# Kernel optimization log

Hardware: AMD Instinct MI355X
Metric: run time of the kernel (lower is better)

Reference implementation:

```python
import jax, jax.numpy as jnp
import numpy as np

GAMMA = 0.96875
ROPE_THETA = 10000.0


def _rope(x):
    # x: (B, S, d) -> rotary applied over interleaved pairs (torchtune-style)
    B, S, d = x.shape
    inv_freq = 1.0 / (ROPE_THETA ** (jnp.arange(0, d, 2, dtype=jnp.float32) / d))  # (d/2,)
    angles = jnp.arange(S, dtype=jnp.float32)[:, None] * inv_freq[None, :]  # (S, d/2)
    cos = jnp.cos(angles).astype(x.dtype)
    sin = jnp.sin(angles).astype(x.dtype)
    xs = x.reshape(B, S, d // 2, 2)
    x0, x1 = xs[..., 0], xs[..., 1]
    out = jnp.stack([x0 * cos - x1 * sin, x1 * cos + x0 * sin], axis=-1)
    return out.reshape(B, S, d)


def _decay_mask(S, dtype):
    n = jnp.arange(S)[:, None]
    m = jnp.arange(S)[None, :]
    diff = n - m
    # gamma^(n-m) for n>=m else 0; clamp exponent to avoid inf/nan
    D = jnp.exp(jnp.maximum(diff, 0).astype(jnp.float32) * np.log(GAMMA))
    return jnp.where(diff >= 0, D, 0.0).astype(dtype)


def setup_inputs() -> dict:
    key = jax.random.key(0)
    k1, k2, k3, k4 = jax.random.split(key, 4)
    H = 256
    X = jax.random.normal(k1, (4, 8192, H), dtype=jnp.float32)
    W_Q = jax.random.normal(k2, (H, H), dtype=jnp.float32) / H
    W_K = jax.random.normal(k3, (H, H), dtype=jnp.float32) / H
    W_V = jax.random.normal(k4, (H, H), dtype=jnp.float32) / H
    return {"X": X, "W_Q": W_Q, "W_K": W_K, "W_V": W_V}


def reference(X, W_Q, W_K, W_V):
    B, S, _ = X.shape
    D = _decay_mask(S, X.dtype)  # (S, S)
    Q = _rope(X @ W_Q)  # (B, S, d)
    K = _rope(X @ W_K)
    V = X @ W_V  # (B, S, v_dim)
    ret = jnp.einsum('bqd,bkd->bqk', Q, K) * D[None]  # (B, S, S)
    return ret @ V
```

## Files before the change

### kernel.cpp

```cpp
#include <hip/hip_runtime.h>
#include <hip/hip_bf16.h>

#define B_  4
#define S_  8192
#define H_  256
#define C_  128
#define NC_ 64
#define M_  (B_*S_)

typedef unsigned short u16;
typedef __attribute__((ext_vector_type(8))) short short8;
typedef __attribute__((ext_vector_type(4))) float f32x4;
typedef __attribute__((address_space(1))) void gas_t;
typedef __attribute__((address_space(3))) void las_t;

static constexpr float L2G   = -0.045803690f;
static constexpr float ROPE2 = -0.103810253f;

__device__ __forceinline__ u16 f2b(float x) {
  union { __hip_bfloat16 b; u16 u; } c; c.b = __float2bfloat16(x); return c.u;
}
__device__ __forceinline__ float b2f(u16 u) {
  union { u16 u; __hip_bfloat16 b; } c; c.u = u; return __bfloat162float(c.b);
}
__device__ __forceinline__ f32x4 mfma16(short8 a, short8 b, f32x4 c) {
  return __builtin_amdgcn_mfma_f32_16x16x32_bf16(a, b, c, 0, 0, 0);
}

__device__ __forceinline__ short8 fr32(const u16* base, int row, int slot) {
  return *reinterpret_cast<const short8*>(base + row*256 + (((slot&24)|((slot&7)^(row&7)))<<3));
}
__device__ __forceinline__ short8 fr16(const u16* base, int row, int slot) {
  return *reinterpret_cast<const short8*>(base + row*128 + (((slot&8)|((slot&7)^(row&7)))<<3));
}
__device__ __forceinline__ short8 fr4(const u16* base, int row, int slot) {
  return *reinterpret_cast<const short8*>(base + row*32 + ((slot ^ (row&3))<<3));
}
__device__ __forceinline__ short8 fragr(const u16* lds, int row, int slot) {
  return *reinterpret_cast<const short8*>(lds + row*64 + ((slot ^ (row & 7)) << 3));
}

__device__ __forceinline__ void stageA(const u16* __restrict__ src, int stride,
                                       u16* smbase, int off, int t) {
  #pragma unroll
  for (int it = 0; it < 4; ++it) {
    const int u = it*256 + t, row = u >> 3, lsl = (u & 7) ^ (row & 7);
    const u16* gp = src + (size_t)row*stride + lsl*8;
    u16* lp = smbase + off + it*2048 + (t & 192)*8;
    __builtin_amdgcn_global_load_lds((gas_t*)gp, (las_t*)lp, 16, 0, 0);
  }
}
__device__ __forceinline__ void stageW(const u16* __restrict__ src, u16* dst, int t) {
  #pragma unroll
  for (int it = 0; it < 2; ++it) {
    const int u = it*512 + t, row = u >> 2, p = u & 3, s = p ^ (row & 3);
    const u16* gp = src + (size_t)row*256 + s*8;
    u16* lp = dst + (size_t)(it*512 + (t & ~63))*8;
    __builtin_amdgcn_global_load_lds((gas_t*)gp, (las_t*)lp, 16, 0, 0);
  }
}

__global__ __launch_bounds__(256) void prep(
    const float* __restrict__ Wq, const float* __restrict__ Wk,
    const float* __restrict__ Wv, u16* __restrict__ WhT, float* __restrict__ RTab)
{
  const int bid = blockIdx.x;
  if (bid < 96) {
    const int i = bid*256 + threadIdx.x;
    const int z = i >> 13, r = i & 8191;
    const int n = r >> 5, k0 = (r & 31) << 3;
    const float* W = (z == 0) ? Wq : (z == 1) ? Wk : Wv;
    u16 o[8];
    #pragma unroll
    for (int j = 0; j < 8; ++j) o[j] = f2b(W[(size_t)(k0 + j)*H_ + n]);
    *reinterpret_cast<uint4*>(WhT + ((size_t)z << 16) + n*H_ + k0) =
        *reinterpret_cast<uint4*>(o);
    return;
  }
  const int i = (bid - 96)*256 + threadIdx.x;
  const int s = i >> 7, h = i & 127;
  const float invf = exp2f(ROPE2 * (float)h);
  float sn, cs;
  sincosf((float)s * invf, &sn, &cs);
  *reinterpret_cast<float2*>(RTab + 2*((size_t)s*128 + h)) = make_float2(cs, sn);
}

__global__ __launch_bounds__(512, 2) void fused_chunk(
    const float* __restrict__ X, const u16* __restrict__ WhT,
    const float* __restrict__ RTab,
    u16* __restrict__ Qh, u16* __restrict__ Tt, float* __restrict__ Oloc)
{
  __shared__ u16 SM[81920];
  u16* XS = SM;
  u16* WB = SM + 32768;
  u16* RB = SM + 49152;
  const int t = threadIdx.x, l = t & 63, wid = t >> 6;
  const int g = l >> 4, l15 = l & 15;
  const int mr = wid >> 2, nq = wid & 3;
  const int c = blockIdx.x, b = blockIdx.y;
  const float* Xc = X + ((size_t)(b*S_ + c*C_))*H_;
  const float4* RT4 = reinterpret_cast<const float4*>(RTab);

  stageW(WhT + 0, WB, t);
  #pragma unroll
  for (int it = 0; it < 8; ++it) {
    const int u = it*512 + t, row = u >> 5, sl = u & 31;
    const float* p = Xc + (size_t)row*256 + sl*8;
    float4 a = *reinterpret_cast<const float4*>(p);
    float4 bb = *reinterpret_cast<const float4*>(p + 4);
    u16 o[8] = {f2b(a.x), f2b(a.y), f2b(a.z), f2b(a.w),
                f2b(bb.x), f2b(bb.y), f2b(bb.z), f2b(bb.w)};
    *reinterpret_cast<uint4*>(XS + row*256 + (((sl&24)|((sl&7)^(row&7)))<<3)) =
        *reinterpret_cast<uint4*>(o);
  }
  __syncthreads();

  f32x4 qa[4][4] = {};
  for (int ks = 0; ks < 8; ++ks) {
    const u16* Wcur = WB + (ks&1)*8192;
    if (ks < 7) stageW(WhT + (ks+1)*32, WB + ((ks+1)&1)*8192, t);
    short8 a[4], bw[4];
    #pragma unroll
    for (int i = 0; i < 4; ++i) a[i] = fr32(XS, mr*64 + i*16 + l15, ks*4 + g);
    #pragma unroll
    for (int j = 0; j < 4; ++j) bw[j] = fr4(Wcur, nq*64 + j*16 + l15, g);
    #pragma unroll
    for (int i = 0; i < 4; ++i)
      #pragma unroll
      for (int j = 0; j < 4; ++j)
        qa[i][j] = mfma16(bw[j], a[i], qa[i][j]);
    __syncthreads();
  }
  #pragma unroll
  for (int i = 0; i < 4; ++i) {
    const int s = c*C_ + mr*64 + i*16 + l15;
    #pragma unroll
    for (int j = 0; j < 4; ++j) {
      const int n0 = nq*64 + j*16 + g*4;
      const float4 tb = RT4[(size_t)s*64 + (n0 >> 2)];
      const float x0 = qa[i][j][0], x1 = qa[i][j][1];
      const float x2 = qa[i][j][2], x3 = qa[i][j][3];
      qa[i][j][0] = x0*tb.x - x1*tb.y;  qa[i][j][1] = x1*tb.x + x0*tb.y;
      qa[i][j][2] = x2*tb.z - x3*tb.w;  qa[i][j][3] = x3*tb.z + x2*tb.w;
    }
  }
  #pragma unroll
  for (int i = 0; i < 4; ++i) {
    const int m = mr*64 + i*16 + l15;
    #pragma unroll
    for (int j = 0; j < 4; ++j) {
      const int n0 = nq*64 + j*16 + g*4;
      ushort4 pk;
      pk.x = f2b(qa[i][j][0]); pk.y = f2b(qa[i][j][1]);
      pk.z = f2b(qa[i][j][2]); pk.w = f2b(qa[i][j][3]);
      const int sl = n0 >> 3;
      *reinterpret_cast<ushort4*>(RB + m*256 + (((sl&24)|((sl&7)^(m&7)))<<3) + (n0&7)) = pk;
    }
  }
  __syncthreads();
  #pragma unroll
  for (int it = 0; it < 8; ++it) {
    const int u = it*512 + t, row = u >> 5, sl = u & 31;
    uint4 v = *reinterpret_cast<const uint4*>(RB + row*256 + (((sl&24)|((sl&7)^(row&7)))<<3));
    *reinterpret_cast<uint4*>(Qh + ((size_t)(b*S_ + c*C_ + row))*H_ + sl*8) = v;
  }

  f32x4 ka[4][4] = {};
  stageW(WhT + 65536, WB, t);
  __syncthreads();
  for (int ks = 0; ks < 8; ++ks) {
    const u16* Wcur = WB + (ks&1)*8192;
    if (ks < 7) stageW(WhT + 65536 + (ks+1)*32, WB + ((ks+1)&1)*8192, t);
    short8 a[4], bw[4];
    #pragma unroll
    for (int i = 0; i < 4; ++i) a[i] = fr32(XS, mr*64 + i*16 + l15, ks*4 + g);
    #pragma unroll
    for (int j = 0; j < 4; ++j) bw[j] = fr4(Wcur, nq*64 + j*16 + l15, g);
    #pragma unroll
    for (int i = 0; i < 4; ++i)
      #pragma unroll
      for (int j = 0; j < 4; ++j)
        ka[i][j] = mfma16(bw[j], a[i], ka[i][j]);
    __syncthreads();
  }
  #pragma unroll
  for (int i = 0; i < 4; ++i) {
    const int s = c*C_ + mr*64 + i*16 + l15;
    #pragma unroll
    for (int j = 0; j < 4; ++j) {
      const int n0 = nq*64 + j*16 + g*4;
      const float4 tb = RT4[(size_t)s*64 + (n0 >> 2)];
      const float x0 = ka[i][j][0], x1 = ka[i][j][1];
      const float x2 = ka[i][j][2], x3 = ka[i][j][3];
      ka[i][j][0] = x0*tb.x - x1*tb.y;  ka[i][j][1] = x1*tb.x + x0*tb.y;
      ka[i][j][2] = x2*tb.z - x3*tb.w;  ka[i][j][3] = x3*tb.z + x2*tb.w;
    }
  }

  const int smh = wid >> 2, sn0 = (wid & 3)*32;
  f32x4 sc[4][2] = {};
  #pragma unroll
  for (int h = 0; h < 2; ++h) {
    if (((wid >> 1) & 1) == h) {
      #pragma unroll
      for (int i = 0; i < 4; ++i) {
        const int m = mr*64 + i*16 + l15;
        #pragma unroll
        for (int j = 0; j < 4; ++j) {
          const int dl0 = (nq&1)*64 + j*16 + g*4;
          ushort4 pk;
          pk.x = f2b(ka[i][j][0]); pk.y = f2b(ka[i][j][1]);
          pk.z = f2b(ka[i][j][2]); pk.w = f2b(ka[i][j][3]);
          const int sl = dl0 >> 3;
          *reinterpret_cast<ushort4*>(WB + m*128 + (((sl&8)|((sl&7)^(m&7)))<<3) + (dl0&7)) = pk;
        }
      }
    }
    __syncthreads();
    #pragma unroll
    for (int kk = 0; kk < 4; ++kk) {
      short8 fa[4], fb[2];
      #pragma unroll
      for (int i = 0; i < 4; ++i) fa[i] = fr16(WB, smh*64 + i*16 + l15, kk*4 + g);
      #pragma unroll
      for (int j = 0; j < 2; ++j) fb[j] = fr32(RB, sn0 + j*16 + l15, h*16 + kk*4 + g);
      #pragma unroll
      for (int i = 0; i < 4; ++i)
        #pragma unroll
        for (int j = 0; j < 2; ++j)
          sc[i][j] = mfma16(fa[i], fb[j], sc[i][j]);
    }
    __syncthreads();
  }
  #pragma unroll
  for (int j = 0; j < 2; ++j) {
    const int n = sn0 + j*16 + l15;
    #pragma unroll
    for (int i = 0; i < 4; ++i) {
      const int m0 = smh*64 + i*16 + g*4;
      ushort4 pk;
      #pragma unroll
      for (int r = 0; r < 4; ++r) {
        const int m = m0 + r;
        const float sv = (n >= m) ? sc[i][j][r] * exp2f((float)(n - m)*L2G) : 0.f;
        reinterpret_cast<u16*>(&pk)[r] = f2b(sv);
      }
      const int sl = m0 >> 3;
      *reinterpret_cast<ushort4*>(WB + n*128 + (((sl&8)|((sl&7)^(n&7)))<<3) + (m0&7)) = pk;
    }
  }
  __syncthreads();

  f32x4 va[4][4] = {};
  stageW(WhT + 2*65536, RB, t);
  __syncthreads();
  for (int ks = 0; ks < 8; ++ks) {
    const u16* Wcur = RB + (ks&1)*8192;
    if (ks < 7) stageW(WhT + 2*65536 + (ks+1)*32, RB + ((ks+1)&1)*8192, t);
    short8 a[4], bw[4];
    #pragma unroll
    for (int i = 0; i < 4; ++i) a[i] = fr32(XS, mr*64 + i*16 + l15, ks*4 + g);
    #pragma unroll
    for (int j = 0; j < 4; ++j) bw[j] = fr4(Wcur, nq*64 + j*16 + l15, g);
    #pragma unroll
    for (int i = 0; i < 4; ++i)
      #pragma unroll
      for (int j = 0; j < 4; ++j)
        va[i][j] = mfma16(a[i], bw[j], va[i][j]);
    __syncthreads();
  }

  #pragma unroll
  for (int jj = 0; jj < 4; ++jj) {
    const int j = nq*64 + jj*16 + l15;
    #pragma unroll
    for (int i = 0; i < 4; ++i) {
      const int m0 = mr*64 + i*16 + g*4;
      ushort4 pk;
      pk.x = f2b(va[i][jj][0]); pk.y = f2b(va[i][jj][1]);
      pk.z = f2b(va[i][jj][2]); pk.w = f2b(va[i][jj][3]);
      const int sl = m0 >> 3;
      *reinterpret_cast<ushort4*>(RB + j*128 + (((sl&8)|((sl&7)^(j&7)))<<3) + (m0&7)) = pk;
    }
  }
  #pragma unroll
  for (int i = 0; i < 4; ++i) {
    const int m = mr*64 + i*16 + l15;
    const float w = exp2f((float)(C_ - 1 - m)*L2G);
    const int slm = m >> 3;
    #pragma unroll
    for (int jj = 0; jj < 4; ++jj) {
      #pragma unroll
      for (int r = 0; r < 4; ++r) {
        const int d = nq*64 + jj*16 + g*4 + r;
        XS[d*128 + (((slm&8)|((slm&7)^(d&7)))<<3) + (m&7)] = f2b(ka[i][jj][r] * w);
      }
    }
  }
  __syncthreads();

  const int ih = wid & 1, jq = wid >> 1;
  {
    f32x4 tt[8][4] = {};
    #pragma unroll
    for (int kk = 0; kk < 4; ++kk) {
      short8 fk[8], fv[4];
      #pragma unroll
      for (int ii = 0; ii < 8; ++ii) fk[ii] = fr16(XS, ih*128 + ii*16 + l15, kk*4 + g);
      #pragma unroll
      for (int jj = 0; jj < 4; ++jj) fv[jj] = fr16(RB, jq*64 + jj*16 + l15, kk*4 + g);
      #pragma unroll
      for (int ii = 0; ii < 8; ++ii)
        #pragma unroll
        for (int jj = 0; jj < 4; ++jj)
          tt[ii][jj] = mfma16(fk[ii], fv[jj], tt[ii][jj]);
    }
    __syncthreads();
    const size_t tb = ((size_t)(b*NC_ + c)) << 16;
    #pragma unroll
    for (int p = 0; p < 2; ++p) {
      if ((jq >> 1) == p) {
        #pragma unroll
        for (int ii = 0; ii < 8; ++ii)
          #pragma unroll
          for (int jj = 0; jj < 4; ++jj) {
            const int jl = (jq&1)*64 + jj*16 + l15;
            const int i0 = ih*128 + ii*16 + g*4;
            ushort4 pk;
            pk.x = f2b(tt[ii][jj][0]); pk.y = f2b(tt[ii][jj][1]);
            pk.z = f2b(tt[ii][jj][2]); pk.w = f2b(tt[ii][jj][3]);
            const int sl = i0 >> 3;
            *reinterpret_cast<ushort4*>(XS + jl*256 + (((sl&24)|((sl&7)^(jl&7)))<<3) + (i0&7)) = pk;
          }
      }
      __syncthreads();
      #pragma unroll
      for (int it = 0; it < 8; ++it) {
        const int u = it*512 + t, row = u >> 5, sl = u & 31;
        uint4 v = *reinterpret_cast<const uint4*>(XS + row*256 + (((sl&24)|((sl&7)^(row&7)))<<3));
        *reinterpret_cast<uint4*>(Tt + tb + (size_t)(p*128 + row)*256 + sl*8) = v;
      }
      __syncthreads();
    }
  }

  {
    f32x4 oa[4][4] = {};
    const int ojq = wid >> 1, onh = wid & 1;
    #pragma unroll
    for (int kk = 0; kk < 4; ++kk) {
      short8 fv[4], fs[4];
      #pragma unroll
      for (int jj = 0; jj < 4; ++jj) fv[jj] = fr16(RB, ojq*64 + jj*16 + l15, kk*4 + g);
      #pragma unroll
      for (int nn = 0; nn < 4; ++nn) fs[nn] = fr16(WB, onh*64 + nn*16 + l15, kk*4 + g);
      #pragma unroll
      for (int jj = 0; jj < 4; ++jj)
        #pragma unroll
        for (int nn = 0; nn < 4; ++nn)
          oa[jj][nn] = mfma16(fv[jj], fs[nn], oa[jj][nn]);
    }
    __syncthreads();
    float* RBf = reinterpret_cast<float*>(RB);
    #pragma unroll
    for (int p = 0; p < 2; ++p) {
      if (onh == p) {
        #pragma unroll
        for (int jj = 0; jj < 4; ++jj)
          #pragma unroll
          for (int nn = 0; nn < 4; ++nn) {
            const int nl = nn*16 + l15;
            const int j0 = ojq*64 + jj*16 + g*4;
            const int sl = j0 >> 2;
            *reinterpret_cast<f32x4*>(RBf + nl*256 + (((sl&56)|((sl&7)^(nl&7)))<<2)) = oa[jj][nn];
          }
      }
      __syncthreads();
      #pragma unroll
      for (int it = 0; it < 8; ++it) {
        const int u = it*512 + t, nl = u >> 6, sl = u & 63;
        f32x4 v = *reinterpret_cast<const f32x4*>(RBf + nl*256 + (((sl&56)|((sl&7)^(nl&7)))<<2));
        *reinterpret_cast<f32x4*>(Oloc + ((size_t)(b*S_ + c*C_ + p*64 + nl))*256 + sl*4) = v;
      }
      __syncthreads();
    }
  }
}

__global__ __launch_bounds__(256) void scan_state(u16* __restrict__ Tt)
{
  const unsigned e = blockIdx.x*256u + threadIdx.x;
  const unsigned b = e >> 15, el = (e & 32767u) << 1;
  const float gC = exp2f(128.0f * L2G);
  float r0 = 0.f, r1 = 0.f;
  const size_t base = (((size_t)b * NC_) << 16) + el;
  #pragma unroll
  for (int grp = 0; grp < 4; ++grp) {
    unsigned buf[16];
    #pragma unroll
    for (int i2 = 0; i2 < 16; ++i2)
      buf[i2] = *reinterpret_cast<const unsigned*>(Tt + base + (size_t)(grp*16 + i2)*65536);
    #pragma unroll
    for (int i2 = 0; i2 < 16; ++i2) {
      const unsigned v = buf[i2];
      *reinterpret_cast<unsigned*>(Tt + base + (size_t)(grp*16 + i2)*65536) =
          (unsigned)f2b(r0) | ((unsigned)f2b(r1) << 16);
      r0 = fmaf(gC, r0, b2f((u16)(v & 0xffff)));
      r1 = fmaf(gC, r1, b2f((u16)(v >> 16)));
    }
  }
}

__global__ __launch_bounds__(256) void cross_out(
    const u16* __restrict__ Qh, const u16* __restrict__ Tt,
    const float* __restrict__ Oloc, float* __restrict__ Out)
{
  __shared__ u16 SM[32768];
  const int t = threadIdx.x, l = t & 63, wid = t >> 6;
  const int wr = wid >> 1, wc = wid & 1, g = l >> 4, l15 = l & 15;
  const int c = blockIdx.x, b = blockIdx.y, jh = blockIdx.z;
  const u16* Asrc = Qh + (size_t)(b*S_ + c*C_)*H_;
  const u16* Bsrc = Tt + (((size_t)(b*NC_ + c)) << 16) + (size_t)(jh*128)*H_;
  f32x4 acc[4][4] = {};

  stageA(Asrc, H_, SM, 0, t);
  stageA(Bsrc, H_, SM, 8192, t);
  __syncthreads();
  for (int ks = 0; ks < 4; ++ks) {
    const int cur = (ks & 1) * 16384;
    if (ks < 3) {
      stageA(Asrc + (ks+1)*64, H_, SM, 16384 - cur, t);
      stageA(Bsrc + (ks+1)*64, H_, SM, 16384 - cur + 8192, t);
    }
    #pragma unroll
    for (int kb = 0; kb < 2; ++kb) {
      short8 fq[4], ft[4];
      #pragma unroll
      for (int i = 0; i < 4; ++i) fq[i] = fragr(SM + cur, wr*64 + i*16 + l15, kb*4 + g);
      #pragma unroll
      for (int j = 0; j < 4; ++j) ft[j] = fragr(SM + cur + 8192, wc*64 + j*16 + l15, kb*4 + g);
      #pragma unroll
      for (int i = 0; i < 4; ++i)
        #pragma unroll
        for (int j = 0; j < 4; ++j)
          acc[i][j] = mfma16(ft[j], fq[i], acc[i][j]);
    }
    __syncthreads();
  }
  #pragma unroll
  for (int i = 0; i < 4; ++i) {
    const float gn = exp2f((float)(wr*64 + i*16 + l15 + 1) * L2G);
    #pragma unroll
    for (int j = 0; j < 4; ++j)
      #pragma unroll
      for (int r = 0; r < 4; ++r) acc[i][j][r] *= gn;
  }
  float* OL = reinterpret_cast<float*>(SM);
  for (int ph = 0; ph < 2; ++ph) {
    if (wr == ph) {
      #pragma unroll
      for (int i = 0; i < 4; ++i) {
        const int nl = i*16 + l15;
        #pragma unroll
        for (int j = 0; j < 4; ++j) {
          const int j0 = wc*64 + j*16 + g*4;
          const int sl = j0 >> 2;
          *reinterpret_cast<f32x4*>(OL + nl*128 + (((sl&24)|((sl&7)^(nl&7)))<<2)) = acc[i][j];
        }
      }
    }
    __syncthreads();
    #pragma unroll
    for (int it = 0; it < 8; ++it) {
      const int u = it*256 + t, nl = u >> 5, sl = u & 31;
      f32x4 v = *reinterpret_cast<const f32x4*>(OL + nl*128 + (((sl&24)|((sl&7)^(nl&7)))<<2));
      const size_t off = ((size_t)(b*S_ + c*C_ + ph*64 + nl))*256 + jh*128 + sl*4;
      f32x4 o = *reinterpret_cast<const f32x4*>(Oloc + off);
      v += o;
      *reinterpret_cast<f32x4*>(Out + off) = v;
    }
    __syncthreads();
  }
}

extern "C" void kernel_launch(void* const* d_in, const int* in_sizes, int n_in,
                              void* d_out, int out_size, void* d_ws, size_t ws_size,
                              hipStream_t stream) {
  const float* X  = (const float*)d_in[0];
  const float* Wq = (const float*)d_in[1];
  const float* Wk = (const float*)d_in[2];
  const float* Wv = (const float*)d_in[3];
  float* Out = (float*)d_out;
  u16* ws = (u16*)d_ws;
  u16*   WhT  = ws;
  float* RTab = (float*)(ws + 196608);
  u16*   Qh   = ws + 196608 + 4194304;
  u16*   Tt   = Qh + (size_t)M_*H_;
  float* Oloc = (float*)(Tt + (size_t)B_*NC_*65536);

  prep<<<96 + 4096, 256, 0, stream>>>(Wq, Wk, Wv, WhT, RTab);
  fused_chunk<<<dim3(NC_, B_), 512, 0, stream>>>(X, WhT, RTab, Qh, Tt, Oloc);
  scan_state<<<(B_*32768)/256, 256, 0, stream>>>(Tt);
  cross_out<<<dim3(NC_, B_, 2), 256, 0, stream>>>(Qh, Tt, Oloc, Out);
}
```

Measured before the change: 86.19 us.

## Move intra-chunk score×V product into output kernel, drop fp32 Oloc round trip

The intra-chunk product (decayed scores times V) is no longer computed in fused_chunk and written as an fp32 Oloc buffer. Instead, fused_chunk writes the bf16 score tile and transposed V tile to global memory. The output kernel then accumulates that product onto the cross-chunk accumulator before storing. This removes the fp32 Oloc write and read plus the staging work in fused_chunk, in exchange for smaller bf16 global intermediates and extra MFMA work in the output kernel. It also changes the W swizzle to sw4 to reduce LDS bank conflicts and drops one barrier.

Measured after the change: 82.77 us. -4.0%, faster.

```diff
diff --git a/kernel.cpp b/kernel.cpp
--- a/kernel.cpp
+++ b/kernel.cpp
@@ -27,6 +27,7 @@
   return __builtin_amdgcn_mfma_f32_16x16x32_bf16(a, b, c, 0, 0, 0);
 }
 
+__device__ __forceinline__ int sw4(int row) { return (row ^ (row >> 2)) & 3; }
 __device__ __forceinline__ short8 fr32(const u16* base, int row, int slot) {
   return *reinterpret_cast<const short8*>(base + row*256 + (((slot&24)|((slot&7)^(row&7)))<<3));
 }
@@ -34,7 +35,7 @@
   return *reinterpret_cast<const short8*>(base + row*128 + (((slot&8)|((slot&7)^(row&7)))<<3));
 }
 __device__ __forceinline__ short8 fr4(const u16* base, int row, int slot) {
-  return *reinterpret_cast<const short8*>(base + row*32 + ((slot ^ (row&3))<<3));
+  return *reinterpret_cast<const short8*>(base + row*32 + ((slot ^ sw4(row))<<3));
 }
 __device__ __forceinline__ short8 fragr(const u16* lds, int row, int slot) {
   return *reinterpret_cast<const short8*>(lds + row*64 + ((slot ^ (row & 7)) << 3));
@@ -53,7 +54,7 @@
 __device__ __forceinline__ void stageW(const u16* __restrict__ src, u16* dst, int t) {
   #pragma unroll
   for (int it = 0; it < 2; ++it) {
-    const int u = it*512 + t, row = u >> 2, p = u & 3, s = p ^ (row & 3);
+    const int u = it*512 + t, row = u >> 2, p = u & 3, s = p ^ sw4(row);
     const u16* gp = src + (size_t)row*256 + s*8;
     u16* lp = dst + (size_t)(it*512 + (t & ~63))*8;
     __builtin_amdgcn_global_load_lds((gas_t*)gp, (las_t*)lp, 16, 0, 0);
@@ -88,7 +89,8 @@
 __global__ __launch_bounds__(512, 2) void fused_chunk(
     const float* __restrict__ X, const u16* __restrict__ WhT,
     const float* __restrict__ RTab,
-    u16* __restrict__ Qh, u16* __restrict__ Tt, float* __restrict__ Oloc)
+    u16* __restrict__ Qh, u16* __restrict__ Tt,
+    u16* __restrict__ Scg, u16* __restrict__ VTg)
 {
   __shared__ u16 SM[81920];
   u16* XS = SM;
@@ -249,7 +251,6 @@
       *reinterpret_cast<ushort4*>(WB + n*128 + (((sl&8)|((sl&7)^(n&7)))<<3) + (m0&7)) = pk;
     }
   }
-  __syncthreads();
 
   f32x4 va[4][4] = {};
   stageW(WhT + 2*65536, RB, t);
@@ -268,6 +269,16 @@
       for (int j = 0; j < 4; ++j)
         va[i][j] = mfma16(a[i], bw[j], va[i][j]);
     __syncthreads();
+  }
+
+  {
+    const size_t scb = ((size_t)(b*NC_ + c)) << 14;
+    #pragma unroll
+    for (int it = 0; it < 4; ++it) {
+      const int u = it*512 + t, row = u >> 4, sl = u & 15;
+      uint4 v = *reinterpret_cast<const uint4*>(WB + row*128 + (((sl&8)|((sl&7)^(row&7)))<<3));
+      *reinterpret_cast<uint4*>(Scg + scb + (size_t)row*128 + sl*8) = v;
+    }
   }
 
   #pragma unroll
@@ -316,6 +327,17 @@
           tt[ii][jj] = mfma16(fk[ii], fv[jj], tt[ii][jj]);
     }
     __syncthreads();
+
+    {
+      const size_t vtb = ((size_t)(b*NC_ + c)) << 15;
+      #pragma unroll
+      for (int it = 0; it < 8; ++it) {
+        const int u = it*512 + t, row = u >> 4, sl = u & 15;
+        uint4 v = *reinterpret_cast<const uint4*>(RB + row*128 + (((sl&8)|((sl&7)^(row&7)))<<3));
+        *reinterpret_cast<uint4*>(VTg + vtb + (size_t)row*128 + sl*8) = v;
+      }
+    }
+
     const size_t tb = ((size_t)(b*NC_ + c)) << 16;
     #pragma unroll
     for (int p = 0; p < 2; ++p) {
@@ -343,48 +365,6 @@
       __syncthreads();
     }
   }
-
-  {
-    f32x4 oa[4][4] = {};
-    const int ojq = wid >> 1, onh = wid & 1;
-    #pragma unroll
-    for (int kk = 0; kk < 4; ++kk) {
-      short8 fv[4], fs[4];
-      #pragma unroll
-      for (int jj = 0; jj < 4; ++jj) fv[jj] = fr16(RB, ojq*64 + jj*16 + l15, kk*4 + g);
-      #pragma unroll
-      for (int nn = 0; nn < 4; ++nn) fs[nn] = fr16(WB, onh*64 + nn*16 + l15, kk*4 + g);
-      #pragma unroll
-      for (int jj = 0; jj < 4; ++jj)
-        #pragma unroll
-        for (int nn = 0; nn < 4; ++nn)
-          oa[jj][nn] = mfma16(fv[jj], fs[nn], oa[jj][nn]);
-    }
-    __syncthreads();
-    float* RBf = reinterpret_cast<float*>(RB);
-    #pragma unroll
-    for (int p = 0; p < 2; ++p) {
-      if (onh == p) {
-        #pragma unroll
-        for (int jj = 0; jj < 4; ++jj)
-          #pragma unroll
-          for (int nn = 0; nn < 4; ++nn) {
-            const int nl = nn*16 + l15;
-            const int j0 = ojq*64 + jj*16 + g*4;
-            const int sl = j0 >> 2;
-            *reinterpret_cast<f32x4*>(RBf + nl*256 + (((sl&56)|((sl&7)^(nl&7)))<<2)) = oa[jj][nn];
-          }
-      }
-      __syncthreads();
-      #pragma unroll
-      for (int it = 0; it < 8; ++it) {
-        const int u = it*512 + t, nl = u >> 6, sl = u & 63;
-        f32x4 v = *reinterpret_cast<const f32x4*>(RBf + nl*256 + (((sl&56)|((sl&7)^(nl&7)))<<2));
-        *reinterpret_cast<f32x4*>(Oloc + ((size_t)(b*S_ + c*C_ + p*64 + nl))*256 + sl*4) = v;
-      }
-      __syncthreads();
-    }
-  }
 }
 
 __global__ __launch_bounds__(256) void scan_state(u16* __restrict__ Tt)
@@ -411,9 +391,10 @@
   }
 }
 
-__global__ __launch_bounds__(256) void cross_out(
+__global__ __launch_bounds__(256) void out_kernel(
     const u16* __restrict__ Qh, const u16* __restrict__ Tt,
-    const float* __restrict__ Oloc, float* __restrict__ Out)
+    const u16* __restrict__ Scg, const u16* __restrict__ VTg,
+    float* __restrict__ Out)
 {
   __shared__ u16 SM[32768];
   const int t = threadIdx.x, l = t & 63, wid = t >> 6;
@@ -447,6 +428,13 @@
     }
     __syncthreads();
   }
+
+  const u16* ScC = Scg + (((size_t)(b*NC_ + c)) << 14);
+  const u16* VtC = VTg + (((size_t)(b*NC_ + c)) << 15) + (size_t)(jh*128)*128;
+  stageA(ScC,      128, SM, 0,     t);
+  stageA(VtC,      128, SM, 8192,  t);
+  stageA(ScC + 64, 128, SM, 16384, t);
+  stageA(VtC + 64, 128, SM, 24576, t);
   #pragma unroll
   for (int i = 0; i < 4; ++i) {
     const float gn = exp2f((float)(wr*64 + i*16 + l15 + 1) * L2G);
@@ -455,6 +443,28 @@
       #pragma unroll
       for (int r = 0; r < 4; ++r) acc[i][j][r] *= gn;
   }
+  __syncthreads();
+
+  #pragma unroll
+  for (int ks2 = 0; ks2 < 2; ++ks2) {
+    #pragma unroll
+    for (int kb = 0; kb < 2; ++kb) {
+      short8 fs[4], fv[4];
+      #pragma unroll
+      for (int i = 0; i < 4; ++i)
+        fs[i] = fragr(SM + ks2*16384, wr*64 + i*16 + l15, kb*4 + g);
+      #pragma unroll
+      for (int j = 0; j < 4; ++j)
+        fv[j] = fragr(SM + ks2*16384 + 8192, wc*64 + j*16 + l15, kb*4 + g);
+      #pragma unroll
+      for (int i = 0; i < 4; ++i)
+        #pragma unroll
+        for (int j = 0; j < 4; ++j)
+          acc[i][j] = mfma16(fv[j], fs[i], acc[i][j]);
+    }
+  }
+  __syncthreads();
+
   float* OL = reinterpret_cast<float*>(SM);
   for (int ph = 0; ph < 2; ++ph) {
     if (wr == ph) {
@@ -475,8 +485,6 @@
       const int u = it*256 + t, nl = u >> 5, sl = u & 31;
       f32x4 v = *reinterpret_cast<const f32x4*>(OL + nl*128 + (((sl&24)|((sl&7)^(nl&7)))<<2));
       const size_t off = ((size_t)(b*S_ + c*C_ + ph*64 + nl))*256 + jh*128 + sl*4;
-      f32x4 o = *reinterpret_cast<const f32x4*>(Oloc + off);
-      v += o;
       *reinterpret_cast<f32x4*>(Out + off) = v;
     }
     __syncthreads();
@@ -496,10 +504,11 @@
   float* RTab = (float*)(ws + 196608);
   u16*   Qh   = ws + 196608 + 4194304;
   u16*   Tt   = Qh + (size_t)M_*H_;
-  float* Oloc = (float*)(Tt + (size_t)B_*NC_*65536);
+  u16*   Scg  = Tt + (size_t)B_*NC_*65536;
+  u16*   VTg  = Scg + (size_t)B_*NC_*16384;
 
   prep<<<96 + 4096, 256, 0, stream>>>(Wq, Wk, Wv, WhT, RTab);
-  fused_chunk<<<dim3(NC_, B_), 512, 0, stream>>>(X, WhT, RTab, Qh, Tt, Oloc);
+  fused_chunk<<<dim3(NC_, B_), 512, 0, stream>>>(X, WhT, RTab, Qh, Tt, Scg, VTg);
   scan_state<<<(B_*32768)/256, 256, 0, stream>>>(Tt);
-  cross_out<<<dim3(NC_, B_, 2), 256, 0, stream>>>(Qh, Tt, Oloc, Out);
-}
+  out_kernel<<<dim3(NC_, B_, 2), 256, 0, stream>>>(Qh, Tt, Scg, VTg, Out);
+}
```
